# Kernel tuning notes

Hardware: AMD Instinct MI355X
Metric: run time of the kernel (lower is better)

Reference implementation:

```python
import jax, jax.numpy as jnp
import numpy as np

N = 100000
C = 128
E = 1600000


def setup_inputs() -> dict:
    key = jax.random.key(0)
    k1, k2, k3, k4 = jax.random.split(key, 4)
    x = jax.random.normal(k1, (N, C), dtype=jnp.float32)
    edge_index = jax.random.randint(k2, (2, E), 0, N, dtype=jnp.int64)
    left_right_idx = jax.random.randint(k3, (E,), 0, E, dtype=jnp.int64)
    # torch.nn.Linear(2C, 1, bias=False) weight: [1, 2C]
    W = jax.random.normal(k4, (1, 2 * C), dtype=jnp.float32) * (1.0 / np.sqrt(2 * C))
    return {"x": x, "edge_index": edge_index, "left_right_idx": left_right_idx, "W": W}


def reference(x, edge_index, left_right_idx, W):
    row, col = edge_index[0], edge_index[1]
    x_row = x[row]            # [E, C]
    x_col = x[col]            # [E, C]
    # linear1(cat([x_row, x_col], -1)) == x_row @ W[:, :C].T + x_col @ W[:, C:].T
    w_row = W[0, :C]          # [C]
    w_col = W[0, C:]          # [C]
    scores = jnp.einsum('ec,c->e', x_row, w_row) + jnp.einsum('ec,c->e', x_col, w_col)  # [E]
    weights = jax.nn.sigmoid(scores)                       # [E]
    edge_weights = weights * weights[left_right_idx]       # [E]
    return edge_weights
```

## Files before the change

### kernel.cpp

```cpp
#include <hip/hip_runtime.h>

#define N_NODES 100000
#define C_DIM   128
#define E_EDGES 1600000

typedef int   i4 __attribute__((ext_vector_type(4)));
typedef float f4 __attribute__((ext_vector_type(4)));

__device__ float g_s_row[N_NODES];
__device__ float g_s_col[N_NODES];

__global__ void node_dots_kernel(const float* __restrict__ x,
                                 const float* __restrict__ W) {
    const int lane = threadIdx.x & 31;
    const int node = blockIdx.x * 8 + (threadIdx.x >> 5);
    if (node >= N_NODES) return;

    const f4 xv = *reinterpret_cast<const f4*>(x + (size_t)node * C_DIM + lane * 4);
    const f4 wr = *reinterpret_cast<const f4*>(W + lane * 4);
    const f4 wc = *reinterpret_cast<const f4*>(W + C_DIM + lane * 4);

    float pr = xv.x * wr.x + xv.y * wr.y + xv.z * wr.z + xv.w * wr.w;
    float pc = xv.x * wc.x + xv.y * wc.y + xv.z * wc.z + xv.w * wc.w;

    #pragma unroll
    for (int off = 16; off > 0; off >>= 1) {
        pr += __shfl_down(pr, off, 32);
        pc += __shfl_down(pc, off, 32);
    }
    if (lane == 0) {
        g_s_row[node] = pr;
        g_s_col[node] = pc;
    }
}

__device__ __forceinline__ float sigmoid_of_edge(const int* __restrict__ ei, int e) {
    const int r = ei[e];
    const int c = ei[E_EDGES + e];
    const float s = g_s_row[r] + g_s_col[c];
    return 1.0f / (1.0f + expf(-s));
}

__global__ void edge_fused_kernel(const int* __restrict__ ei,
                                  const int* __restrict__ lr,
                                  float* __restrict__ out) {
    const int e = (blockIdx.x * blockDim.x + threadIdx.x) * 4;
    if (e >= E_EDGES) return;

    const i4 r4 = *reinterpret_cast<const i4*>(ei + e);
    const i4 c4 = *reinterpret_cast<const i4*>(ei + E_EDGES + e);
    const i4 l4 = __builtin_nontemporal_load(reinterpret_cast<const i4*>(lr + e));

    const float s0 = g_s_row[r4.x] + g_s_col[c4.x];
    const float s1 = g_s_row[r4.y] + g_s_col[c4.y];
    const float s2 = g_s_row[r4.z] + g_s_col[c4.z];
    const float s3 = g_s_row[r4.w] + g_s_col[c4.w];

    const float w0 = 1.0f / (1.0f + expf(-s0));
    const float w1 = 1.0f / (1.0f + expf(-s1));
    const float w2 = 1.0f / (1.0f + expf(-s2));
    const float w3 = 1.0f / (1.0f + expf(-s3));

    const float p0 = sigmoid_of_edge(ei, l4.x);
    const float p1 = sigmoid_of_edge(ei, l4.y);
    const float p2 = sigmoid_of_edge(ei, l4.z);
    const float p3 = sigmoid_of_edge(ei, l4.w);

    f4 o;
    o.x = w0 * p0;
    o.y = w1 * p1;
    o.z = w2 * p2;
    o.w = w3 * p3;
    __builtin_nontemporal_store(o, reinterpret_cast<f4*>(out + e));
}

extern "C" void kernel_launch(void* const* d_in, const int* in_sizes, int n_in,
                              void* d_out, int out_size, void* d_ws, size_t ws_size,
                              hipStream_t stream) {
    const float* x  = (const float*)d_in[0];
    const int*   ei = (const int*)d_in[1];
    const int*   lr = (const int*)d_in[2];
    const float* W  = (const float*)d_in[3];
    float* out = (float*)d_out;

    node_dots_kernel<<<(N_NODES + 7) / 8, 256, 0, stream>>>(x, W);

    const int threads_e = E_EDGES / 4;
    edge_fused_kernel<<<(threads_e + 255) / 256, 256, 0, stream>>>(ei, lr, out);
}
```

Before: 162.4 us.

## Split edge kernel into sigmoid pass and paired multiply pass

The fused edge kernel is split into two passes. The first computes each edge's sigmoid weight into a workspace buffer. The second multiplies each weight by the weight gathered at left_right_idx. Before, the partner's weight was recomputed with three dependent random gathers (row index, col index, then the two node scores); now it is a single random 4-byte gather from a 6.4MB buffer. The cost is an extra kernel launch and a 6.4MB write and read round trip through the workspace.

```diff
diff --git a/kernel.cpp b/kernel.cpp
--- a/kernel.cpp
+++ b/kernel.cpp
@@ -34,43 +34,41 @@
     }
 }
 
-__device__ __forceinline__ float sigmoid_of_edge(const int* __restrict__ ei, int e) {
-    const int r = ei[e];
-    const int c = ei[E_EDGES + e];
-    const float s = g_s_row[r] + g_s_col[c];
-    return 1.0f / (1.0f + expf(-s));
-}
-
-__global__ void edge_fused_kernel(const int* __restrict__ ei,
-                                  const int* __restrict__ lr,
-                                  float* __restrict__ out) {
+__global__ void edge_sigmoid_kernel(const int* __restrict__ ei,
+                                    float* __restrict__ wts) {
     const int e = (blockIdx.x * blockDim.x + threadIdx.x) * 4;
     if (e >= E_EDGES) return;
 
-    const i4 r4 = *reinterpret_cast<const i4*>(ei + e);
-    const i4 c4 = *reinterpret_cast<const i4*>(ei + E_EDGES + e);
-    const i4 l4 = __builtin_nontemporal_load(reinterpret_cast<const i4*>(lr + e));
+    const i4 r4 = __builtin_nontemporal_load(reinterpret_cast<const i4*>(ei + e));
+    const i4 c4 = __builtin_nontemporal_load(reinterpret_cast<const i4*>(ei + E_EDGES + e));
 
     const float s0 = g_s_row[r4.x] + g_s_col[c4.x];
     const float s1 = g_s_row[r4.y] + g_s_col[c4.y];
     const float s2 = g_s_row[r4.z] + g_s_col[c4.z];
     const float s3 = g_s_row[r4.w] + g_s_col[c4.w];
 
-    const float w0 = 1.0f / (1.0f + expf(-s0));
-    const float w1 = 1.0f / (1.0f + expf(-s1));
-    const float w2 = 1.0f / (1.0f + expf(-s2));
-    const float w3 = 1.0f / (1.0f + expf(-s3));
+    f4 w;
+    w.x = 1.0f / (1.0f + expf(-s0));
+    w.y = 1.0f / (1.0f + expf(-s1));
+    w.z = 1.0f / (1.0f + expf(-s2));
+    w.w = 1.0f / (1.0f + expf(-s3));
+    *reinterpret_cast<f4*>(wts + e) = w;
+}
 
-    const float p0 = sigmoid_of_edge(ei, l4.x);
-    const float p1 = sigmoid_of_edge(ei, l4.y);
-    const float p2 = sigmoid_of_edge(ei, l4.z);
-    const float p3 = sigmoid_of_edge(ei, l4.w);
+__global__ void pair_mul_kernel(const float* __restrict__ wts,
+                                const int* __restrict__ lr,
+                                float* __restrict__ out) {
+    const int e = (blockIdx.x * blockDim.x + threadIdx.x) * 4;
+    if (e >= E_EDGES) return;
+
+    const i4 l4 = __builtin_nontemporal_load(reinterpret_cast<const i4*>(lr + e));
+    const f4 w4 = *reinterpret_cast<const f4*>(wts + e);
 
     f4 o;
-    o.x = w0 * p0;
-    o.y = w1 * p1;
-    o.z = w2 * p2;
-    o.w = w3 * p3;
+    o.x = w4.x * wts[l4.x];
+    o.y = w4.y * wts[l4.y];
+    o.z = w4.z * wts[l4.z];
+    o.w = w4.w * wts[l4.w];
     __builtin_nontemporal_store(o, reinterpret_cast<f4*>(out + e));
 }
 
@@ -83,8 +81,11 @@
     const float* W  = (const float*)d_in[3];
     float* out = (float*)d_out;
 
+    float* wts = (float*)d_ws;
+
     node_dots_kernel<<<(N_NODES + 7) / 8, 256, 0, stream>>>(x, W);
 
     const int threads_e = E_EDGES / 4;
-    edge_fused_kernel<<<(threads_e + 255) / 256, 256, 0, stream>>>(ei, lr, out);
+    edge_sigmoid_kernel<<<(threads_e + 255) / 256, 256, 0, stream>>>(ei, wts);
+    pair_mul_kernel<<<(threads_e + 255) / 256, 256, 0, stream>>>(wts, lr, out);
 }
```

After: 133.2 us. -18.0%, faster.
